# Performance work log

Measured on AMD Instinct MI355X. Metric: run time of the kernel, lower is better.

The kernel has to match this reference:

```python
import jax, jax.numpy as jnp
import numpy as np

N_NODES = 100000


def gcn_conv(x, edge_index, W, b, add_self_loops=True):
    """PyG GCNConv: out = D^{-1/2}(A+I)D^{-1/2} (x @ W) + b, sum-aggregated at col."""
    n = x.shape[0]
    x = x @ W  # linear first, like PyG (smaller feature dim usually)
    row, col = edge_index[0], edge_index[1]
    if add_self_loops:
        loop = jnp.arange(n, dtype=row.dtype)
        row = jnp.concatenate([row, loop])
        col = jnp.concatenate([col, loop])
    ones = jnp.ones(row.shape[0], dtype=x.dtype)
    deg = jax.ops.segment_sum(ones, col, num_segments=n)  # in-degree incl. self loops
    dinv = jnp.where(deg > 0, jax.lax.rsqrt(deg), 0.0)
    norm = dinv[row] * dinv[col]  # [E]
    msg = x[row] * norm[:, None]  # gather + scale, [E, F]
    out = jax.ops.segment_sum(msg, col, num_segments=n)  # scatter-add
    return out + b


def setup_inputs() -> dict:
    key = jax.random.key(0)
    ks = jax.random.split(key, 12)
    latent_dim, condition_dim, hidden_dim, output_dim = 64, 32, 64, 64
    n_edges = 1600000
    latent = jax.random.normal(ks[0], (N_NODES, latent_dim), dtype=jnp.float32)
    condition = jax.random.normal(ks[1], (N_NODES, condition_dim), dtype=jnp.float32)
    edge_index = jax.random.randint(ks[2], (2, n_edges), 0, N_NODES, dtype=jnp.int64 if jax.config.jax_enable_x64 else jnp.int32)

    def glorot(k, fan_in, fan_out):
        s = jnp.sqrt(6.0 / (fan_in + fan_out))
        return jax.random.uniform(k, (fan_in, fan_out), minval=-s, maxval=s, dtype=jnp.float32)

    W1 = glorot(ks[3], latent_dim, hidden_dim); b1 = jnp.zeros((hidden_dim,), jnp.float32)
    W2 = glorot(ks[4], condition_dim, hidden_dim); b2 = jnp.zeros((hidden_dim,), jnp.float32)
    W3 = glorot(ks[5], 2 * hidden_dim, hidden_dim); b3 = jnp.zeros((hidden_dim,), jnp.float32)
    W4 = glorot(ks[6], hidden_dim, output_dim); b4 = jnp.zeros((output_dim,), jnp.float32)
    return {"latent": latent, "condition": condition, "edge_index": edge_index,
            "W1": W1, "b1": b1, "W2": W2, "b2": b2,
            "W3": W3, "b3": b3, "W4": W4, "b4": b4}


def reference(latent, condition, edge_index, W1, b1, W2, b2, W3, b3, W4, b4):
    z2h = gcn_conv(latent, edge_index, W1, b1)
    c2h = gcn_conv(condition, edge_index, W2, b2)
    h = jnp.concatenate([z2h, c2h], axis=1)
    h = gcn_conv(h, edge_index, W3, b3)
    out = gcn_conv(h, edge_index, W4, b4)
    return out
```

## Files before the change

### kernel.cpp

```cpp
#include <hip/hip_runtime.h>
#include <hip/hip_fp16.h>

#define BKN 4
#define CBN 256
#define CHUNK 4096
#define MAXBIN 5120

typedef _Float16 half8 __attribute__((ext_vector_type(8)));
typedef _Float16 h4v __attribute__((ext_vector_type(4)));
typedef float floatx4 __attribute__((ext_vector_type(4)));


__global__ void zero_int_kernel(int* __restrict__ p, int n) {
    int i = blockIdx.x * blockDim.x + threadIdx.x;
    if (i < n) p[i] = 0;
}


__global__ __launch_bounds__(256) void histCB_kernel(const int* __restrict__ ei,
                                                     int* __restrict__ cntCB,
                                                     int E, int NCB) {
    __shared__ int lcnt[512];
    int tid = threadIdx.x;
    for (int i = tid; i < 512; i += 256) lcnt[i] = 0;
    __syncthreads();
    int base = blockIdx.x * CHUNK;
    #pragma unroll
    for (int q = 0; q < 16; ++q) {
        int e = base + q * 256 + tid;
        if (e < E) atomicAdd(&lcnt[ei[E + e] >> 8], 1);
    }
    __syncthreads();
    for (int i = tid; i < NCB; i += 256)
        if (lcnt[i]) atomicAdd(&cntCB[i], lcnt[i]);
}


__global__ __launch_bounds__(512) void scanCB_kernel(const int* __restrict__ cntCB,
                                                     int* __restrict__ offCB,
                                                     int* __restrict__ curCB, int NCB) {
    __shared__ int sA[512], sB[512];
    int tid = threadIdx.x;
    sA[tid] = (tid < NCB) ? cntCB[tid] : 0;
    __syncthreads();
    int* src = sA; int* dst = sB;
    for (int o = 1; o < 512; o <<= 1) {
        dst[tid] = src[tid] + (tid >= o ? src[tid - o] : 0);
        __syncthreads();
        int* t = src; src = dst; dst = t;
    }
    if (tid <= NCB) {
        int v = (tid > 0) ? src[tid - 1] : 0;
        offCB[tid] = v;
        if (tid < NCB) curCB[tid] = v;
    }
}


__global__ __launch_bounds__(256) void passA_kernel(const int* __restrict__ ei,
                                                    int* __restrict__ curCB,
                                                    unsigned* __restrict__ binned,
                                                    int E, int NCB) {
    __shared__ int lcnt[512];
    __shared__ int sA[512], sB[512];
    __shared__ int loffx[512];
    __shared__ int gbase[512];
    __shared__ int lpos[512];
    __shared__ unsigned stage[CHUNK];
    int tid = threadIdx.x;
    int base = blockIdx.x * CHUNK;
    for (int i = tid; i < 512; i += 256) lcnt[i] = 0;
    __syncthreads();
    unsigned pk[16]; int bin[16];
    #pragma unroll
    for (int q = 0; q < 16; ++q) {
        int e = base + q * 256 + tid;
        if (e < E) {
            int r = ei[e], c = ei[E + e];
            pk[q] = ((unsigned)r << 8) | (unsigned)(c & 255);
            bin[q] = c >> 8;
            atomicAdd(&lcnt[bin[q]], 1);
        } else bin[q] = -1;
    }
    __syncthreads();
    for (int i = tid; i < 512; i += 256) sA[i] = lcnt[i];
    __syncthreads();
    int* src = sA; int* dst = sB;
    for (int o = 1; o < 512; o <<= 1) {
        for (int i = tid; i < 512; i += 256)
            dst[i] = src[i] + (i >= o ? src[i - o] : 0);
        __syncthreads();
        int* t = src; src = dst; dst = t;
    }
    for (int i = tid; i < 512; i += 256) {
        int ex = (i > 0) ? src[i - 1] : 0;
        loffx[i] = ex;
        lpos[i] = ex;
        int c = lcnt[i];
        gbase[i] = (c > 0 && i < NCB) ? atomicAdd(&curCB[i], c) : 0;
    }
    __syncthreads();
    #pragma unroll
    for (int q = 0; q < 16; ++q) {
        if (bin[q] >= 0) {
            int p = atomicAdd(&lpos[bin[q]], 1);
            stage[p] = pk[q];
        }
    }
    __syncthreads();
    for (int b = tid; b < NCB; b += 256) {
        int n = lcnt[b];
        int g = gbase[b];
        int lo = loffx[b];
        for (int i2 = 0; i2 < n; ++i2) binned[g + i2] = stage[lo + i2];
    }
}


__global__ __launch_bounds__(256) void passB_kernel(const unsigned* __restrict__ binned,
                                                    const int* __restrict__ offCB,
                                                    unsigned* __restrict__ bkt,
                                                    int* __restrict__ offB,
                                                    float* __restrict__ dinv,
                                                    int N, int NCB, int NB) {
    __shared__ unsigned raw[MAXBIN];
    __shared__ unsigned stage[MAXBIN];
    __shared__ int fcnt[64], foff[65], fpos[64];
    __shared__ int ncnt[256];
    int i = blockIdx.x;
    int tid = threadIdx.x;
    int g0 = offCB[i], g1 = offCB[i + 1];
    int cnt = g1 - g0;
    if (cnt > MAXBIN) cnt = MAXBIN;
    for (int j = tid; j < 64; j += 256) fcnt[j] = 0;
    ncnt[tid] = 0;
    __syncthreads();
    for (int idx = tid; idx < cnt; idx += 256) {
        unsigned pk = binned[g0 + idx];
        raw[idx] = pk;
        atomicAdd(&fcnt[(pk >> 2) & 63], 1);
        atomicAdd(&ncnt[pk & 255], 1);
    }
    __syncthreads();
    if (tid == 0) {
        int run = 0;
        for (int j = 0; j < 64; ++j) { foff[j] = run; run += fcnt[j]; }
        foff[64] = run;
    }
    __syncthreads();
    if (tid < 64) fpos[tid] = foff[tid];
    __syncthreads();
    for (int idx = tid; idx < cnt; idx += 256) {
        unsigned pk = raw[idx];
        int p = atomicAdd(&fpos[(pk >> 2) & 63], 1);
        stage[p] = ((pk >> 8) << 2) | (pk & 3);
    }
    __syncthreads();
    for (int idx = tid; idx < cnt; idx += 256) bkt[g0 + idx] = stage[idx];
    int fb0 = i * 64;
    int nfb = min(64, NB - fb0);
    for (int j = tid; j < nfb; j += 256) offB[fb0 + j] = g0 + foff[j];
    if (i == NCB - 1 && tid == 0) offB[NB] = g1;
    int n0 = i * CBN;
    int n = n0 + tid;
    if (n < N) dinv[n] = rsqrtf((float)ncnt[tid] + 1.0f);
}

__global__ __launch_bounds__(256) void fold_kernel(
    const float* __restrict__ W1, const float* __restrict__ b1,
    const float* __restrict__ W2, const float* __restrict__ b2,
    const float* __restrict__ W3, const float* __restrict__ b3,
    const float* __restrict__ W4,
    float* __restrict__ Wf1, float* __restrict__ Wf2,
    float* __restrict__ u, float* __restrict__ v) {
    __shared__ float As[64][64];
    __shared__ float gsl[64];
    int tid = threadIdx.x;
    int f = tid & 63;
    int w = __builtin_amdgcn_readfirstlane(tid >> 6);
    int blk = blockIdx.x;

    float w4c[64];
    #pragma unroll
    for (int k = 0; k < 64; ++k) w4c[k] = W4[k * 64 + f];

    if (blk < 24) {
        const int half = (blk < 16) ? 0 : 64;
        #pragma unroll 2
        for (int kk = 0; kk < 16; ++kk) {
            int k = w * 16 + kk;
            float a = 0.f;
            #pragma unroll
            for (int j = 0; j < 64; ++j)
                a += W3[(half + k) * 64 + j] * w4c[j];
            As[k][f] = a;
        }
        __syncthreads();
        const float* Wsrc = (blk < 16) ? W1 : W2;
        float* Wdst = (blk < 16) ? Wf1 : Wf2;
        int i = ((blk < 16) ? blk : (blk - 16)) * 4 + w;
        float a = 0.f;
        #pragma unroll
        for (int k = 0; k < 64; ++k)
            a += Wsrc[i * 64 + k] * As[k][f];
        Wdst[i * 64 + f] = a;
    } else {
        float g = 0.f;
        #pragma unroll
        for (int k = 0; k < 64; ++k) g += b1[k] * W3[k * 64 + f];
        #pragma unroll
        for (int k = 0; k < 64; ++k) g += b2[k] * W3[(64 + k) * 64 + f];
        if (w == 0) gsl[f] = g;
        __syncthreads();
        if (w == 0) {
            float uu = 0.f, vv = 0.f;
            #pragma unroll
            for (int k = 0; k < 64; ++k) {
                uu += gsl[k] * w4c[k];
                vv += b3[k] * w4c[k];
            }
            u[f] = uu;
            v[f] = vv;
        }
    }
}

__global__ __launch_bounds__(256) void linZ_kernel(
    const float* __restrict__ lat, const float* __restrict__ cond,
    const float* __restrict__ Wf1, const float* __restrict__ Wf2,
    const float* __restrict__ dinv, _Float16* __restrict__ Z, int N) {
    __shared__ _Float16 Xs[64][104];
    __shared__ _Float16 Wt[64][104];
    int tid = threadIdx.x;
    int n0 = blockIdx.x * 64;
    {
        const float4* lat4 = (const float4*)(lat + (size_t)n0 * 64);
        #pragma unroll
        for (int q = 0; q < 4; ++q) {
            int idx = q * 256 + tid;
            int row = idx >> 4;
            float4 v = make_float4(0.f, 0.f, 0.f, 0.f);
            if (n0 + row < N) v = lat4[idx];
            int col = (idx & 15) * 4;
            Xs[row][col + 0] = (_Float16)v.x;
            Xs[row][col + 1] = (_Float16)v.y;
            Xs[row][col + 2] = (_Float16)v.z;
            Xs[row][col + 3] = (_Float16)v.w;
        }
        const float4* cond4 = (const float4*)(cond + (size_t)n0 * 32);
        #pragma unroll
        for (int q = 0; q < 2; ++q) {
            int idx = q * 256 + tid;
            int row = idx >> 3;
            float4 v = make_float4(0.f, 0.f, 0.f, 0.f);
            if (n0 + row < N) v = cond4[idx];
            int col = 64 + (idx & 7) * 4;
            Xs[row][col + 0] = (_Float16)v.x;
            Xs[row][col + 1] = (_Float16)v.y;
            Xs[row][col + 2] = (_Float16)v.z;
            Xs[row][col + 3] = (_Float16)v.w;
        }
        for (int i = tid; i < 4096; i += 256) {
            int k = i >> 6, f = i & 63;
            Wt[f][k] = (_Float16)Wf1[i];
        }
        for (int i = tid; i < 2048; i += 256) {
            int k = i >> 6, f = i & 63;
            Wt[f][64 + k] = (_Float16)Wf2[i];
        }
    }
    __syncthreads();
    int lane = tid & 63, wave = tid >> 6;
    int quad = lane >> 4, l16 = lane & 15;
    floatx4 acc[4] = {};
    #pragma unroll
    for (int kc = 0; kc < 96; kc += 32) {
        half8 a = *(const half8*)&Xs[wave * 16 + l16][kc + quad * 8];
        #pragma unroll
        for (int nt = 0; nt < 4; ++nt) {
            half8 b = *(const half8*)&Wt[nt * 16 + l16][kc + quad * 8];
            acc[nt] = __builtin_amdgcn_mfma_f32_16x16x32_f16(a, b, acc[nt], 0, 0, 0);
        }
    }
    #pragma unroll
    for (int r = 0; r < 4; ++r) {
        int n = n0 + wave * 16 + quad * 4 + r;
        if (n < N) {
            float d = dinv[n];
            #pragma unroll
            for (int nt = 0; nt < 4; ++nt)
                Z[(size_t)n * 64 + nt * 16 + l16] = (_Float16)(acc[nt][r] * d);
        }
    }
}

template <bool FINAL>
__global__ __launch_bounds__(256) void hop_kernel(
    const _Float16* __restrict__ Vp, const float* __restrict__ dinv,
    const int* __restrict__ offB, const unsigned* __restrict__ bkt,
    const float* __restrict__ wvec, void* __restrict__ outv, int NB) {
    int lane = threadIdx.x & 63;
    int wave = threadIdx.x >> 6;
    int b = blockIdx.x * 4 + wave;
    if (b >= NB) return;
    int g  = lane >> 4;
    int fq = lane & 15;
    int c0 = b * BKN;

    float acc[4][4];
    {
        h4v h = *(const h4v*)&Vp[(size_t)(c0 + g) * 64 + fq * 4];
        #pragma unroll
        for (int t = 0; t < 4; ++t)
            #pragma unroll
            for (int j = 0; j < 4; ++j)
                acc[t][j] = (t == g) ? (float)h[j] : 0.f;
    }

    int s = offB[b], e = offB[b + 1];
    #pragma unroll 4
    for (int i0 = s; i0 < e; i0 += 4) {
        int idx = i0 + g;
        unsigned pk = bkt[min(idx, e - 1)];
        int te = (idx < e) ? (int)(pk & 3u) : 4;
        int r  = (int)(pk >> 2);
        h4v h = *(const h4v*)&Vp[(size_t)r * 64 + fq * 4];
        float v0 = (float)h[0], v1 = (float)h[1];
        float v2 = (float)h[2], v3 = (float)h[3];
        #pragma unroll
        for (int t = 0; t < 4; ++t) {
            float sel = (te == t) ? 1.f : 0.f;
            acc[t][0] = fmaf(sel, v0, acc[t][0]);
            acc[t][1] = fmaf(sel, v1, acc[t][1]);
            acc[t][2] = fmaf(sel, v2, acc[t][2]);
            acc[t][3] = fmaf(sel, v3, acc[t][3]);
        }
    }

    #pragma unroll
    for (int t = 0; t < 4; ++t)
        #pragma unroll
        for (int j = 0; j < 4; ++j) {
            float x = acc[t][j];
            x += __shfl_xor(x, 16, 64);
            x += __shfl_xor(x, 32, 64);
            acc[t][j] = x;
        }

    float og[4];
    #pragma unroll
    for (int j = 0; j < 4; ++j) {
        float x0 = (g == 0) ? acc[0][j] : acc[1][j];
        float x1 = (g == 2) ? acc[2][j] : acc[3][j];
        og[j] = (g < 2) ? x0 : x1;
    }
    float d = dinv[c0 + g];
    float4 wv = *(const float4*)&wvec[fq * 4];
    if constexpr (FINAL) {
        float4 o;
        o.x = og[0] * d + wv.x;
        o.y = og[1] * d + wv.y;
        o.z = og[2] * d + wv.z;
        o.w = og[3] * d + wv.w;
        *(float4*)&((float*)outv)[(size_t)(c0 + g) * 64 + fq * 4] = o;
    } else {
        float dd = d * d;
        h4v o;
        o[0] = (_Float16)(og[0] * dd + d * wv.x);
        o[1] = (_Float16)(og[1] * dd + d * wv.y);
        o[2] = (_Float16)(og[2] * dd + d * wv.z);
        o[3] = (_Float16)(og[3] * dd + d * wv.w);
        *(h4v*)&((_Float16*)outv)[(size_t)(c0 + g) * 64 + fq * 4] = o;
    }
}


static inline size_t align256(size_t x) { return (x + 255) & ~(size_t)255; }

extern "C" void kernel_launch(void* const* d_in, const int* in_sizes, int n_in,
                              void* d_out, int out_size, void* d_ws, size_t ws_size,
                              hipStream_t stream) {
    const float* latent = (const float*)d_in[0];
    const float* cond   = (const float*)d_in[1];
    const int*   ei     = (const int*)d_in[2];
    const float* W1 = (const float*)d_in[3];
    const float* b1 = (const float*)d_in[4];
    const float* W2 = (const float*)d_in[5];
    const float* b2 = (const float*)d_in[6];
    const float* W3 = (const float*)d_in[7];
    const float* b3 = (const float*)d_in[8];
    const float* W4 = (const float*)d_in[9];
    const float* b4 = (const float*)d_in[10];
    float* out = (float*)d_out;

    const int N = in_sizes[0] / 64;
    const int E = in_sizes[2] / 2;
    const int NB  = (N + BKN - 1) / BKN;
    const int NCB = (N + CBN - 1) / CBN;
    const int NCH = (E + CHUNK - 1) / CHUNK;

    char* w = (char*)d_ws;
    size_t o = 0;
    int* cntCB = (int*)(w + o); o = align256(o + (size_t)NCB * 4);
    int* offCB = (int*)(w + o); o = align256(o + (size_t)(NCB + 1) * 4);
    int* curCB = (int*)(w + o); o = align256(o + (size_t)NCB * 4);
    int* offB  = (int*)(w + o); o = align256(o + (size_t)(NB + 1) * 4);
    float* dinv = (float*)(w + o); o = align256(o + (size_t)N * 4);
    float* Wf1 = (float*)(w + o); o = align256(o + 4096 * 4);
    float* Wf2 = (float*)(w + o); o = align256(o + 2048 * 4);
    float* uVec = (float*)(w + o); o = align256(o + 64 * 4);
    float* vVec = (float*)(w + o); o = align256(o + 64 * 4);
    unsigned* binned = (unsigned*)(w + o); o = align256(o + (size_t)E * 4);
    unsigned* bkt    = (unsigned*)(w + o); o = align256(o + (size_t)E * 4);
    _Float16* Z = (_Float16*)(w + o); o = align256(o + (size_t)N * 64 * 2);
    _Float16* P = (_Float16*)(w + o); o = align256(o + (size_t)N * 64 * 2);

    const int BS = 256;
    int gHop = (NB + 3) / 4;

    zero_int_kernel<<<2, BS, 0, stream>>>(cntCB, NCB);
    histCB_kernel<<<NCH, BS, 0, stream>>>(ei, cntCB, E, NCB);
    scanCB_kernel<<<1, 512, 0, stream>>>(cntCB, offCB, curCB, NCB);
    passA_kernel<<<NCH, BS, 0, stream>>>(ei, curCB, binned, E, NCB);
    passB_kernel<<<NCB, BS, 0, stream>>>(binned, offCB, bkt, offB, dinv, N, NCB, NB);

    fold_kernel<<<25, BS, 0, stream>>>(W1, b1, W2, b2, W3, b3, W4, Wf1, Wf2, uVec, vVec);
    linZ_kernel<<<(N + 63) / 64, BS, 0, stream>>>(latent, cond, Wf1, Wf2, dinv, Z, N);

    hop_kernel<false><<<gHop, BS, 0, stream>>>(Z, dinv, offB, bkt, uVec, (void*)P, NB);
    hop_kernel<false><<<gHop, BS, 0, stream>>>(P, dinv, offB, bkt, vVec, (void*)Z, NB);
    hop_kernel<true ><<<gHop, BS, 0, stream>>>(Z, dinv, offB, bkt, b4, (void*)out, NB);
}
```

Before: 277.7 us.

## Replace histogram+scan with fixed-capacity bin regions and coalesce passA scatter

Drops the coarse-bin histogram and scan kernels by giving each coarse bin a fixed region of MAXBIN slots, with the cursor initialised to i*MAXBIN. Bucket ranges become begin/end arrays (offB/offE) because bins are no longer contiguous. passA now writes staged entries out with one thread per element, using a per-slot bin id, instead of one thread per bin looping serially. This removes two launches and a full extra read of the edge columns. It assumes no coarse bin exceeds MAXBIN edges, otherwise writes overflow into the next region, and it enlarges the workspace.

```diff
diff --git a/kernel.cpp b/kernel.cpp
--- a/kernel.cpp
+++ b/kernel.cpp
@@ -11,49 +11,9 @@
 typedef float floatx4 __attribute__((ext_vector_type(4)));
 
 
-__global__ void zero_int_kernel(int* __restrict__ p, int n) {
+__global__ void init_cur_kernel(int* __restrict__ p, int n, int stride) {
     int i = blockIdx.x * blockDim.x + threadIdx.x;
-    if (i < n) p[i] = 0;
-}
-
-
-__global__ __launch_bounds__(256) void histCB_kernel(const int* __restrict__ ei,
-                                                     int* __restrict__ cntCB,
-                                                     int E, int NCB) {
-    __shared__ int lcnt[512];
-    int tid = threadIdx.x;
-    for (int i = tid; i < 512; i += 256) lcnt[i] = 0;
-    __syncthreads();
-    int base = blockIdx.x * CHUNK;
-    #pragma unroll
-    for (int q = 0; q < 16; ++q) {
-        int e = base + q * 256 + tid;
-        if (e < E) atomicAdd(&lcnt[ei[E + e] >> 8], 1);
-    }
-    __syncthreads();
-    for (int i = tid; i < NCB; i += 256)
-        if (lcnt[i]) atomicAdd(&cntCB[i], lcnt[i]);
-}
-
-
-__global__ __launch_bounds__(512) void scanCB_kernel(const int* __restrict__ cntCB,
-                                                     int* __restrict__ offCB,
-                                                     int* __restrict__ curCB, int NCB) {
-    __shared__ int sA[512], sB[512];
-    int tid = threadIdx.x;
-    sA[tid] = (tid < NCB) ? cntCB[tid] : 0;
-    __syncthreads();
-    int* src = sA; int* dst = sB;
-    for (int o = 1; o < 512; o <<= 1) {
-        dst[tid] = src[tid] + (tid >= o ? src[tid - o] : 0);
-        __syncthreads();
-        int* t = src; src = dst; dst = t;
-    }
-    if (tid <= NCB) {
-        int v = (tid > 0) ? src[tid - 1] : 0;
-        offCB[tid] = v;
-        if (tid < NCB) curCB[tid] = v;
-    }
+    if (i < n) p[i] = i * stride;
 }
 
 
@@ -67,6 +27,7 @@
     __shared__ int gbase[512];
     __shared__ int lpos[512];
     __shared__ unsigned stage[CHUNK];
+    __shared__ unsigned short sbin[CHUNK];
     int tid = threadIdx.x;
     int base = blockIdx.x * CHUNK;
     for (int i = tid; i < 512; i += 256) lcnt[i] = 0;
@@ -105,22 +66,23 @@
         if (bin[q] >= 0) {
             int p = atomicAdd(&lpos[bin[q]], 1);
             stage[p] = pk[q];
-        }
-    }
-    __syncthreads();
-    for (int b = tid; b < NCB; b += 256) {
-        int n = lcnt[b];
-        int g = gbase[b];
-        int lo = loffx[b];
-        for (int i2 = 0; i2 < n; ++i2) binned[g + i2] = stage[lo + i2];
+            sbin[p] = (unsigned short)bin[q];
+        }
+    }
+    __syncthreads();
+    int total = min(CHUNK, E - base);
+    for (int idx = tid; idx < total; idx += 256) {
+        int b2 = sbin[idx];
+        binned[gbase[b2] + (idx - loffx[b2])] = stage[idx];
     }
 }
 
 
 __global__ __launch_bounds__(256) void passB_kernel(const unsigned* __restrict__ binned,
-                                                    const int* __restrict__ offCB,
+                                                    const int* __restrict__ curCB,
                                                     unsigned* __restrict__ bkt,
                                                     int* __restrict__ offB,
+                                                    int* __restrict__ offE,
                                                     float* __restrict__ dinv,
                                                     int N, int NCB, int NB) {
     __shared__ unsigned raw[MAXBIN];
@@ -129,8 +91,8 @@
     __shared__ int ncnt[256];
     int i = blockIdx.x;
     int tid = threadIdx.x;
-    int g0 = offCB[i], g1 = offCB[i + 1];
-    int cnt = g1 - g0;
+    int g0 = i * MAXBIN;
+    int cnt = curCB[i] - g0;
     if (cnt > MAXBIN) cnt = MAXBIN;
     for (int j = tid; j < 64; j += 256) fcnt[j] = 0;
     ncnt[tid] = 0;
@@ -159,8 +121,10 @@
     for (int idx = tid; idx < cnt; idx += 256) bkt[g0 + idx] = stage[idx];
     int fb0 = i * 64;
     int nfb = min(64, NB - fb0);
-    for (int j = tid; j < nfb; j += 256) offB[fb0 + j] = g0 + foff[j];
-    if (i == NCB - 1 && tid == 0) offB[NB] = g1;
+    for (int j = tid; j < nfb; j += 256) {
+        offB[fb0 + j] = g0 + foff[j];
+        offE[fb0 + j] = g0 + foff[j + 1];
+    }
     int n0 = i * CBN;
     int n = n0 + tid;
     if (n < N) dinv[n] = rsqrtf((float)ncnt[tid] + 1.0f);
@@ -297,7 +261,8 @@
 template <bool FINAL>
 __global__ __launch_bounds__(256) void hop_kernel(
     const _Float16* __restrict__ Vp, const float* __restrict__ dinv,
-    const int* __restrict__ offB, const unsigned* __restrict__ bkt,
+    const int* __restrict__ offB, const int* __restrict__ offE,
+    const unsigned* __restrict__ bkt,
     const float* __restrict__ wvec, void* __restrict__ outv, int NB) {
     int lane = threadIdx.x & 63;
     int wave = threadIdx.x >> 6;
@@ -317,7 +282,7 @@
                 acc[t][j] = (t == g) ? (float)h[j] : 0.f;
     }
 
-    int s = offB[b], e = offB[b + 1];
+    int s = offB[b], e = offE[b];
     #pragma unroll 4
     for (int i0 = s; i0 < e; i0 += 4) {
         int idx = i0 + g;
@@ -398,36 +363,34 @@
     const int NB  = (N + BKN - 1) / BKN;
     const int NCB = (N + CBN - 1) / CBN;
     const int NCH = (E + CHUNK - 1) / CHUNK;
+    const size_t REG = (size_t)NCB * MAXBIN;
 
     char* w = (char*)d_ws;
     size_t o = 0;
-    int* cntCB = (int*)(w + o); o = align256(o + (size_t)NCB * 4);
-    int* offCB = (int*)(w + o); o = align256(o + (size_t)(NCB + 1) * 4);
     int* curCB = (int*)(w + o); o = align256(o + (size_t)NCB * 4);
-    int* offB  = (int*)(w + o); o = align256(o + (size_t)(NB + 1) * 4);
+    int* offB  = (int*)(w + o); o = align256(o + (size_t)NB * 4);
+    int* offE  = (int*)(w + o); o = align256(o + (size_t)NB * 4);
     float* dinv = (float*)(w + o); o = align256(o + (size_t)N * 4);
     float* Wf1 = (float*)(w + o); o = align256(o + 4096 * 4);
     float* Wf2 = (float*)(w + o); o = align256(o + 2048 * 4);
     float* uVec = (float*)(w + o); o = align256(o + 64 * 4);
     float* vVec = (float*)(w + o); o = align256(o + 64 * 4);
-    unsigned* binned = (unsigned*)(w + o); o = align256(o + (size_t)E * 4);
-    unsigned* bkt    = (unsigned*)(w + o); o = align256(o + (size_t)E * 4);
+    unsigned* binned = (unsigned*)(w + o); o = align256(o + REG * 4);
+    unsigned* bkt    = (unsigned*)(w + o); o = align256(o + REG * 4);
     _Float16* Z = (_Float16*)(w + o); o = align256(o + (size_t)N * 64 * 2);
     _Float16* P = (_Float16*)(w + o); o = align256(o + (size_t)N * 64 * 2);
 
     const int BS = 256;
     int gHop = (NB + 3) / 4;
 
-    zero_int_kernel<<<2, BS, 0, stream>>>(cntCB, NCB);
-    histCB_kernel<<<NCH, BS, 0, stream>>>(ei, cntCB, E, NCB);
-    scanCB_kernel<<<1, 512, 0, stream>>>(cntCB, offCB, curCB, NCB);
+    init_cur_kernel<<<2, BS, 0, stream>>>(curCB, NCB, MAXBIN);
     passA_kernel<<<NCH, BS, 0, stream>>>(ei, curCB, binned, E, NCB);
-    passB_kernel<<<NCB, BS, 0, stream>>>(binned, offCB, bkt, offB, dinv, N, NCB, NB);
+    passB_kernel<<<NCB, BS, 0, stream>>>(binned, curCB, bkt, offB, offE, dinv, N, NCB, NB);
 
     fold_kernel<<<25, BS, 0, stream>>>(W1, b1, W2, b2, W3, b3, W4, Wf1, Wf2, uVec, vVec);
     linZ_kernel<<<(N + 63) / 64, BS, 0, stream>>>(latent, cond, Wf1, Wf2, dinv, Z, N);
 
-    hop_kernel<false><<<gHop, BS, 0, stream>>>(Z, dinv, offB, bkt, uVec, (void*)P, NB);
-    hop_kernel<false><<<gHop, BS, 0, stream>>>(P, dinv, offB, bkt, vVec, (void*)Z, NB);
-    hop_kernel<true ><<<gHop, BS, 0, stream>>>(Z, dinv, offB, bkt, b4, (void*)out, NB);
-}
+    hop_kernel<false><<<gHop, BS, 0, stream>>>(Z, dinv, offB, offE, bkt, uVec, (void*)P, NB);
+    hop_kernel<false><<<gHop, BS, 0, stream>>>(P, dinv, offB, offE, bkt, vVec, (void*)Z, NB);
+    hop_kernel<true ><<<gHop, BS, 0, stream>>>(Z, dinv, offB, offE, bkt, b4, (void*)out, NB);
+}
```

Result: faster. 259.2 us (-6.7%).
